# Optimization experiments

Measured on AMD Instinct MI355X. Metric: run time of the kernel, lower is better.

## Reference

```python
import jax, jax.numpy as jnp
import numpy as np

BOX_W, GIOU_W, OBJ_W, CLS_W, CTR_W = 5.0, 2.0, 1.0, 1.5, 0.5
POS_RADIUS = 1.0


def _bce_logits(x, t):
    # numerically stable binary cross entropy with logits
    return jnp.maximum(x, 0.0) - x * t + jnp.log1p(jnp.exp(-jnp.abs(x)))


def _focal(logits, targets, alpha=0.25, gamma=2.0):
    p = jax.nn.sigmoid(logits)
    ce = _bce_logits(logits, targets)
    p_t = p * targets + (1.0 - p) * (1.0 - targets)
    a_t = alpha * targets + (1.0 - alpha) * (1.0 - targets)
    return (a_t * ce * (1.0 - p_t) ** gamma).mean()


def _centerness(ltrb):
    l, t, r, b = ltrb[..., 0], ltrb[..., 1], ltrb[..., 2], ltrb[..., 3]
    hor = jnp.minimum(l, r) / jnp.maximum(jnp.maximum(l, r), 1e-6)
    ver = jnp.minimum(t, b) / jnp.maximum(jnp.maximum(t, b), 1e-6)
    return jnp.sqrt(jnp.maximum(hor * ver, 0.0))


def _build_targets(locations, gt_boxes, gt_labels, grid_h, grid_w, num_classes):
    # Vectorized equivalent of the sequential smallest-area-first assignment:
    # each location takes the smallest-area gt among its candidate gts.
    lx, ly = locations[:, 0], locations[:, 1]            # [L]
    cx, cy, w, h = (gt_boxes[..., i] for i in range(4))  # [B,M]
    x1, y1, x2, y2 = cx - w / 2, cy - h / 2, cx + w / 2, cy + h / 2
    area = w * h                                          # [B,M]
    # [B,M,L] booleans
    inside_box = (lx > x1[..., None]) & (ly > y1[..., None]) & (lx < x2[..., None]) & (ly < y2[..., None])
    rx, ry = POS_RADIUS / grid_w, POS_RADIUS / grid_h
    inside_center = (jnp.abs(lx - cx[..., None]) <= rx) & (jnp.abs(ly - cy[..., None]) <= ry)
    candidate = inside_box & inside_center
    # fallback: objects with no candidate grab the closest location (prefer inside-box)
    dist = (lx - cx[..., None]) ** 2 + (ly - cy[..., None]) ** 2
    dist_in = jnp.where(inside_box, dist, jnp.inf)
    best = jnp.where(inside_box.any(-1), jnp.argmin(dist_in, -1), jnp.argmin(dist, -1))  # [B,M]
    L = lx.shape[0]
    fallback = jax.nn.one_hot(best, L, dtype=bool)
    candidate = jnp.where(candidate.any(-1, keepdims=True), candidate, fallback)
    # per-location: pick candidate gt with min area (first index on ties)
    cost = jnp.where(candidate, area[..., None], jnp.inf)   # [B,M,L]
    assigned = jnp.argmin(cost, axis=1)                      # [B,L]
    positive = jnp.isfinite(jnp.min(cost, axis=1))           # [B,L]
    gt_xyxy = jnp.stack([x1, y1, x2, y2], axis=-1)           # [B,M,4]
    abox = jnp.take_along_axis(gt_xyxy, assigned[:, :, None], axis=1)  # [B,L,4]
    ltrb = jnp.stack([lx - abox[..., 0], ly - abox[..., 1], abox[..., 2] - lx, abox[..., 3] - ly], axis=-1)
    ltrb = jnp.maximum(ltrb, 1e-6)
    pos_f = positive.astype(jnp.float32)
    alab = jnp.take_along_axis(gt_labels, assigned, axis=1)  # [B,L]
    cls_t = jax.nn.one_hot(alab, num_classes, dtype=jnp.float32) * pos_f[..., None]
    ctr_t = _centerness(ltrb) * pos_f
    return abox * pos_f[..., None], ltrb * pos_f[..., None], cls_t, pos_f, ctr_t, positive


def _detection_loss(boxes_xyxy, box_deltas, class_logits, objectness, centerness,
                    locations, gt_boxes, gt_labels, grid_h, grid_w):
    C = class_logits.shape[-1]
    box_t, ltrb_t, cls_t, obj_t, ctr_t, positive = _build_targets(
        locations, gt_boxes, gt_labels, grid_h, grid_w, C)
    loss_obj = _focal(objectness, obj_t)
    loss_cls = _focal(class_logits, cls_t)
    # positive-weighted box terms (masked weighted sums over the full grid)
    weights = jnp.where(positive, jnp.maximum(jax.lax.stop_gradient(ctr_t), 0.1), 0.0)  # [B,L]
    wsum = weights.sum()
    # smooth L1 on ltrb deltas, beta=0.1
    beta = 0.1
    d = jnp.abs(box_deltas - ltrb_t)
    l1 = jnp.where(d < beta, 0.5 * d * d / beta, d - 0.5 * beta).mean(-1)  # [B,L]
    loss_l1 = (l1 * weights).sum() / wsum
    # elementwise GIoU between predicted and assigned gt xyxy boxes
    p, g = boxes_xyxy, box_t
    inter_lt = jnp.maximum(p[..., :2], g[..., :2])
    inter_rb = jnp.minimum(p[..., 2:], g[..., 2:])
    inter_wh = jnp.maximum(inter_rb - inter_lt, 0.0)
    inter = inter_wh[..., 0] * inter_wh[..., 1]
    area_p = jnp.maximum(p[..., 2] - p[..., 0], 0.0) * jnp.maximum(p[..., 3] - p[..., 1], 0.0)
    area_g = jnp.maximum(g[..., 2] - g[..., 0], 0.0) * jnp.maximum(g[..., 3] - g[..., 1], 0.0)
    union = area_p + area_g - inter
    iou = inter / jnp.maximum(union, 1e-6)
    hull_lt = jnp.minimum(p[..., :2], g[..., :2])
    hull_rb = jnp.maximum(p[..., 2:], g[..., 2:])
    hull_wh = jnp.maximum(hull_rb - hull_lt, 0.0)
    hull = hull_wh[..., 0] * hull_wh[..., 1]
    giou = iou - (hull - union) / jnp.maximum(hull, 1e-6)
    loss_giou = ((1.0 - giou) * weights).sum() / wsum
    ctr_bce = _bce_logits(centerness, ctr_t)
    loss_ctr = (ctr_bce * weights).sum() / wsum
    return (OBJ_W * loss_obj + CTR_W * loss_ctr + CLS_W * loss_cls
            + BOX_W * loss_l1 + GIOU_W * loss_giou)


def setup_inputs() -> dict:
    key = jax.random.key(0)
    ks = jax.random.split(key, 8)
    B, M, H, W, C = 16, 32, 128, 128, 80
    L = H * W
    ys, xs = jnp.meshgrid(jnp.arange(H, dtype=jnp.float32), jnp.arange(W, dtype=jnp.float32), indexing='ij')
    locations = jnp.stack([(xs + 0.5) / W, (ys + 0.5) / H], axis=-1).reshape(L, 2)
    gt_c = jax.random.uniform(ks[0], (B, M, 2), minval=0.1, maxval=0.9)
    gt_wh = jax.random.uniform(ks[1], (B, M, 2), minval=0.02, maxval=0.3)
    gt_boxes = jnp.concatenate([gt_c, gt_wh], axis=-1)
    gt_labels = jax.random.randint(ks[2], (B, M), 0, C)
    pc = jax.random.uniform(ks[3], (B, L, 2), minval=0.05, maxval=0.95)
    pwh = jax.random.uniform(ks[4], (B, L, 2), minval=0.02, maxval=0.3)
    boxes_xyxy = jnp.concatenate([pc - pwh / 2, pc + pwh / 2], axis=-1)
    box_deltas = jax.random.uniform(ks[5], (B, L, 4), minval=1e-3, maxval=0.3)
    class_logits = jax.random.normal(ks[6], (B, L, C), dtype=jnp.float32)
    k7, k8 = jax.random.split(ks[7])
    objectness = jax.random.normal(k7, (B, L), dtype=jnp.float32)
    centerness = jax.random.normal(k8, (B, L), dtype=jnp.float32)
    return {"boxes_xyxy": boxes_xyxy, "box_deltas": box_deltas, "class_logits": class_logits,
            "objectness": objectness, "centerness": centerness, "locations": locations,
            "gt_boxes": gt_boxes, "gt_labels": gt_labels, "grid_h": H, "grid_w": W}


def reference(boxes_xyxy, box_deltas, class_logits, objectness, centerness,
              locations, gt_boxes, gt_labels, grid_h, grid_w):
    return _detection_loss(boxes_xyxy, box_deltas, class_logits, objectness, centerness,
                           locations, gt_boxes, gt_labels, grid_h, grid_w)
```

## Files before the change

### kernel.cpp

```cpp
#include <hip/hip_runtime.h>
#include <cstdint>
#include <cstddef>
#include <math.h>

#define BOX_W_C  5.0f
#define GIOU_W_C 2.0f
#define OBJ_W_C  1.0f
#define CLS_W_C  1.5f
#define CTR_W_C  0.5f
#define POS_RADIUS_C 1.0f
#define MAXM 128
#define BLK 256

__device__ __forceinline__ float focal_elem(float x, float t) {
    float ax = fabsf(x);
    float e  = __expf(-ax);
    float lg = __logf(1.0f + e);
    float ce = fmaxf(x, 0.0f) - x * t + lg;
    float inv = 1.0f / (1.0f + e);
    float p  = (x >= 0.0f) ? inv : e * inv;
    float p_t = p * t + (1.0f - p) * (1.0f - t);
    float a_t = 0.25f * t + 0.75f * (1.0f - t);
    float om  = 1.0f - p_t;
    return a_t * ce * om * om;
}

__device__ __forceinline__ float focal_neg(float x) {
    float ax = fabsf(x);
    float e  = __expf(-ax);
    float lg = __logf(1.0f + e);
    float ce = fmaxf(x, 0.0f) + lg;
    float inv = 1.0f / (1.0f + e);
    float p  = (x >= 0.0f) ? inv : e * inv;
    return 0.75f * ce * p * p;
}

__device__ __forceinline__ float focal_pos_correction(float x) {
    float ax = fabsf(x);
    float e  = __expf(-ax);
    float lg = __logf(1.0f + e);
    float relu = fmaxf(x, 0.0f);
    float inv = 1.0f / (1.0f + e);
    float p  = (x >= 0.0f) ? inv : e * inv;
    float om = 1.0f - p;
    float f1 = 0.25f * (relu - x + lg) * om * om;
    float f0 = 0.75f * (relu + lg) * p * p;
    return f1 - f0;
}

__global__ void gt_assign_kernel(const float* __restrict__ locations,
                                 const float* __restrict__ gt_boxes,
                                 const int* __restrict__ gh_p,
                                 const int* __restrict__ gw_p,
                                 int L, int M,
                                 float* __restrict__ info,
                                 int* __restrict__ flags) {
    int bm  = blockIdx.x;
    int tid = threadIdx.x;

    const float* gb = gt_boxes + (size_t)bm * 4;
    float cx = gb[0], cy = gb[1], w = gb[2], h = gb[3];
    float x1 = cx - w * 0.5f, y1 = cy - h * 0.5f;
    float x2 = cx + w * 0.5f, y2 = cy + h * 0.5f;
    float area = w * h;
    float rx = POS_RADIUS_C / (float)gw_p[0];
    float ry = POS_RADIUS_C / (float)gh_p[0];

    float bin_v  = INFINITY; int bin_i  = 0x7fffffff;
    float ball_v = INFINITY; int ball_i = 0x7fffffff;
    int any_cand = 0, any_in = 0;

    const float2* loc2 = (const float2*)locations;
    for (int l = tid; l < L; l += blockDim.x) {
        float2 p2 = loc2[l];
        float lx = p2.x, ly = p2.y;
        bool inb = (lx > x1) && (ly > y1) && (lx < x2) && (ly < y2);
        bool inc = (fabsf(lx - cx) <= rx) && (fabsf(ly - cy) <= ry);
        any_cand |= (int)(inb && inc);
        any_in   |= (int)inb;
        float dx = lx - cx, dy = ly - cy;
        float dist = dx * dx + dy * dy;
        if (dist < ball_v) { ball_v = dist; ball_i = l; }
        float din = inb ? dist : INFINITY;
        if (din < bin_v) { bin_v = din; bin_i = l; }
    }

    __shared__ float s_v1[512]; __shared__ int s_i1[512];
    __shared__ float s_v2[512]; __shared__ int s_i2[512];
    __shared__ int s_c[512]; __shared__ int s_n[512];
    s_v1[tid] = bin_v;  s_i1[tid] = bin_i;
    s_v2[tid] = ball_v; s_i2[tid] = ball_i;
    s_c[tid] = any_cand; s_n[tid] = any_in;
    __syncthreads();
    for (int s = blockDim.x / 2; s > 0; s >>= 1) {
        if (tid < s) {
            if (s_v1[tid + s] < s_v1[tid] ||
                (s_v1[tid + s] == s_v1[tid] && s_i1[tid + s] < s_i1[tid])) {
                s_v1[tid] = s_v1[tid + s]; s_i1[tid] = s_i1[tid + s];
            }
            if (s_v2[tid + s] < s_v2[tid] ||
                (s_v2[tid + s] == s_v2[tid] && s_i2[tid + s] < s_i2[tid])) {
                s_v2[tid] = s_v2[tid + s]; s_i2[tid] = s_i2[tid + s];
            }
            s_c[tid] |= s_c[tid + s];
            s_n[tid] |= s_n[tid + s];
        }
        __syncthreads();
    }
    if (tid == 0) {
        int best = s_n[0] ? s_i1[0] : s_i2[0];
        flags[bm * 2]     = s_c[0];
        flags[bm * 2 + 1] = best;
        float* oi = info + (size_t)bm * 8;
        oi[0] = x1; oi[1] = y1; oi[2] = x2; oi[3] = y2;
        oi[4] = cx; oi[5] = cy; oi[6] = area; oi[7] = 0.0f;
    }
}

__global__ void fused_loss_kernel(const float* __restrict__ boxes_xyxy,
                                  const float* __restrict__ box_deltas,
                                  const float* __restrict__ class_logits,
                                  const float* __restrict__ objectness,
                                  const float* __restrict__ centerness,
                                  const float* __restrict__ locations,
                                  const int* __restrict__ gt_labels,
                                  const int* __restrict__ gh_p,
                                  const int* __restrict__ gw_p,
                                  int L, int M, int C, int bpb, int nblk,
                                  const float* __restrict__ info,
                                  const int* __restrict__ flags,
                                  float* __restrict__ partials) {
    __shared__ float s_x1[MAXM], s_y1[MAXM], s_x2[MAXM], s_y2[MAXM];
    __shared__ float s_cx[MAXM], s_cy[MAXM], s_area[MAXM];
    __shared__ int   s_lab[MAXM], s_hc[MAXM], s_best[MAXM];

    int b    = blockIdx.x / bpb;
    int lblk = blockIdx.x % bpb;
    int tid  = threadIdx.x;

    if (tid < M && tid < MAXM) {
        int bm = b * M + tid;
        const float* oi = info + (size_t)bm * 8;
        s_x1[tid] = oi[0]; s_y1[tid] = oi[1]; s_x2[tid] = oi[2]; s_y2[tid] = oi[3];
        s_cx[tid] = oi[4]; s_cy[tid] = oi[5]; s_area[tid] = oi[6];
        s_lab[tid]  = gt_labels[bm];
        s_hc[tid]   = flags[bm * 2];
        s_best[tid] = flags[bm * 2 + 1];
    }
    __syncthreads();

    int l0 = lblk * BLK;
    int l  = l0 + tid;
    float a_obj = 0.f, a_w = 0.f, a_l1 = 0.f, a_giou = 0.f, a_ctr = 0.f;
    float a_cls = 0.f;
    int mylab = -1;

    if (l < L) {
        size_t bl = (size_t)b * L + l;
        const float2* loc2 = (const float2*)locations;
        float2 p2 = loc2[l];
        float lx = p2.x, ly = p2.y;
        float rx = POS_RADIUS_C / (float)gw_p[0];
        float ry = POS_RADIUS_C / (float)gh_p[0];

        float minc = INFINITY;
        int   asg  = -1;
        for (int m = 0; m < M; ++m) {
            bool cand;
            if (s_hc[m]) {
                cand = (lx > s_x1[m]) && (ly > s_y1[m]) && (lx < s_x2[m]) && (ly < s_y2[m])
                    && (fabsf(lx - s_cx[m]) <= rx) && (fabsf(ly - s_cy[m]) <= ry);
            } else {
                cand = (l == s_best[m]);
            }
            if (cand && (s_area[m] < minc)) { minc = s_area[m]; asg = m; }
        }
        bool  pos   = (asg >= 0);
        float pos_f = pos ? 1.0f : 0.0f;
        mylab = pos ? s_lab[asg] : -1;

        a_obj = focal_elem(objectness[bl], pos_f);

        if (pos) {
            float ax1 = s_x1[asg], ay1 = s_y1[asg], ax2 = s_x2[asg], ay2 = s_y2[asg];
            float ltl = fmaxf(lx - ax1, 1e-6f);
            float ltt = fmaxf(ly - ay1, 1e-6f);
            float ltr = fmaxf(ax2 - lx, 1e-6f);
            float ltb = fmaxf(ay2 - ly, 1e-6f);
            float hor = fminf(ltl, ltr) / fmaxf(fmaxf(ltl, ltr), 1e-6f);
            float ver = fminf(ltt, ltb) / fmaxf(fmaxf(ltt, ltb), 1e-6f);
            float ctr_t = sqrtf(fmaxf(hor * ver, 0.0f));
            float wgt = fmaxf(ctr_t, 0.1f);
            a_w = wgt;

            const float4 bd = *(const float4*)(box_deltas + bl * 4);
            float d0 = fabsf(bd.x - ltl), d1 = fabsf(bd.y - ltt);
            float d2 = fabsf(bd.z - ltr), d3 = fabsf(bd.w - ltb);
            float l1s = ((d0 < 0.1f) ? (0.5f * d0 * d0 / 0.1f) : (d0 - 0.05f))
                      + ((d1 < 0.1f) ? (0.5f * d1 * d1 / 0.1f) : (d1 - 0.05f))
                      + ((d2 < 0.1f) ? (0.5f * d2 * d2 / 0.1f) : (d2 - 0.05f))
                      + ((d3 < 0.1f) ? (0.5f * d3 * d3 / 0.1f) : (d3 - 0.05f));
            a_l1 = (l1s * 0.25f) * wgt;

            const float4 pb = *(const float4*)(boxes_xyxy + bl * 4);
            float px1 = pb.x, py1 = pb.y, px2 = pb.z, py2 = pb.w;
            float ilx = fmaxf(px1, ax1), ily = fmaxf(py1, ay1);
            float irx = fminf(px2, ax2), iry = fminf(py2, ay2);
            float iw = fmaxf(irx - ilx, 0.f), ih = fmaxf(iry - ily, 0.f);
            float inter = iw * ih;
            float ap = fmaxf(px2 - px1, 0.f) * fmaxf(py2 - py1, 0.f);
            float ag = fmaxf(ax2 - ax1, 0.f) * fmaxf(ay2 - ay1, 0.f);
            float un = ap + ag - inter;
            float iou = inter / fmaxf(un, 1e-6f);
            float hlx = fminf(px1, ax1), hly = fminf(py1, ay1);
            float hrx = fmaxf(px2, ax2), hry = fmaxf(py2, ay2);
            float hw = fmaxf(hrx - hlx, 0.f), hh = fmaxf(hry - hly, 0.f);
            float hull = hw * hh;
            float giou = iou - (hull - un) / fmaxf(hull, 1e-6f);
            a_giou = (1.0f - giou) * wgt;

            float xc = centerness[bl];
            float bce = fmaxf(xc, 0.f) - xc * ctr_t + __logf(1.0f + __expf(-fabsf(xc)));
            a_ctr = bce * wgt;
        }

        if (mylab >= 0) {
            float xl = class_logits[bl * (size_t)C + mylab];
            a_cls += focal_pos_correction(xl);
        }
    }

    {
        int nrows = L - l0; if (nrows > BLK) nrows = BLK;
        int C4 = C >> 2;
        if (C4 > 0) {
            const float4* cl4 = (const float4*)(class_logits + ((size_t)b * L + l0) * C);
            int total4 = nrows * C4;
            for (int it = tid; it < total4; it += BLK) {
                float4 v = cl4[it];
                a_cls += focal_neg(v.x);
                a_cls += focal_neg(v.y);
                a_cls += focal_neg(v.z);
                a_cls += focal_neg(v.w);
            }
        }
        int crem = C - (C4 << 2);
        if (crem) {
            const float* base = class_logits + ((size_t)b * L + l0) * C + (C4 << 2);
            for (int rr = tid; rr < nrows; rr += BLK)
                for (int j = 0; j < crem; ++j)
                    a_cls += focal_neg(base[(size_t)rr * C + j]);
        }
    }

    for (int off = 32; off > 0; off >>= 1) {
        a_obj  += __shfl_down(a_obj,  off);
        a_w    += __shfl_down(a_w,    off);
        a_l1   += __shfl_down(a_l1,   off);
        a_giou += __shfl_down(a_giou, off);
        a_ctr  += __shfl_down(a_ctr,  off);
        a_cls  += __shfl_down(a_cls,  off);
    }
    __shared__ float red[BLK / 64][6];
    int wid = tid >> 6;
    if ((tid & 63) == 0) {
        red[wid][0] = a_obj; red[wid][1] = a_w; red[wid][2] = a_l1;
        red[wid][3] = a_giou; red[wid][4] = a_ctr; red[wid][5] = a_cls;
    }
    __syncthreads();
    if (tid == 0) {
        float r0 = 0.f, r1 = 0.f, r2 = 0.f, r3 = 0.f, r4 = 0.f, r5 = 0.f;
        for (int w2 = 0; w2 < BLK / 64; ++w2) {
            r0 += red[w2][0]; r1 += red[w2][1]; r2 += red[w2][2];
            r3 += red[w2][3]; r4 += red[w2][4]; r5 += red[w2][5];
        }
        int blk = (int)blockIdx.x;
        partials[0 * nblk + blk] = r0;
        partials[1 * nblk + blk] = r1;
        partials[2 * nblk + blk] = r2;
        partials[3 * nblk + blk] = r3;
        partials[4 * nblk + blk] = r4;
        partials[5 * nblk + blk] = r5;
    }
}

__global__ void finalize_kernel(const float* __restrict__ partials, int nblk,
                                float* __restrict__ out,
                                float invBL, float invBLC) {
    int tid = threadIdx.x;
    float r[6] = {0.f, 0.f, 0.f, 0.f, 0.f, 0.f};
    for (int i = tid; i < nblk; i += blockDim.x) {
        r[0] += partials[0 * nblk + i];
        r[1] += partials[1 * nblk + i];
        r[2] += partials[2 * nblk + i];
        r[3] += partials[3 * nblk + i];
        r[4] += partials[4 * nblk + i];
        r[5] += partials[5 * nblk + i];
    }
    __shared__ float red[256][6];
    for (int j = 0; j < 6; ++j) red[tid][j] = r[j];
    __syncthreads();
    for (int s = (int)blockDim.x / 2; s > 0; s >>= 1) {
        if (tid < s) {
            for (int j = 0; j < 6; ++j) red[tid][j] += red[tid + s][j];
        }
        __syncthreads();
    }
    if (tid == 0) {
        float obj  = red[0][0] * invBL;
        float wsum = red[0][1];
        float l1   = red[0][2] / wsum;
        float giou = red[0][3] / wsum;
        float ctr  = red[0][4] / wsum;
        float cls  = red[0][5] * invBLC;
        out[0] = OBJ_W_C * obj + CTR_W_C * ctr + CLS_W_C * cls + BOX_W_C * l1 + GIOU_W_C * giou;
    }
}

extern "C" void kernel_launch(void* const* d_in, const int* in_sizes, int n_in,
                              void* d_out, int out_size, void* d_ws, size_t ws_size,
                              hipStream_t stream) {
    const float* boxes_xyxy   = (const float*)d_in[0];
    const float* box_deltas   = (const float*)d_in[1];
    const float* class_logits = (const float*)d_in[2];
    const float* objectness   = (const float*)d_in[3];
    const float* centerness   = (const float*)d_in[4];
    const float* locations    = (const float*)d_in[5];
    const float* gt_boxes     = (const float*)d_in[6];
    const int*   gt_labels    = (const int*)d_in[7];
    const int*   gh           = (const int*)d_in[8];
    const int*   gw           = (const int*)d_in[9];

    int L = in_sizes[5] / 2;
    int B = in_sizes[3] / L;
    int C = in_sizes[2] / in_sizes[3];
    int M = in_sizes[7] / B;

    int bpb  = (L + BLK - 1) / BLK;
    int nblk = B * bpb;

    char* p = (char*)d_ws;
    int*   flags  = (int*)p;              p += ((size_t)B * M * 2 * sizeof(int) + 63) / 64 * 64;
    float* info   = (float*)p;            p += ((size_t)B * M * 8 * sizeof(float) + 63) / 64 * 64;
    float* partials = (float*)p;

    gt_assign_kernel<<<B * M, 512, 0, stream>>>(locations, gt_boxes, gh, gw,
                                                L, M, info, flags);

    fused_loss_kernel<<<nblk, BLK, 0, stream>>>(boxes_xyxy, box_deltas,
                                                class_logits, objectness,
                                                centerness, locations,
                                                gt_labels, gh, gw,
                                                L, M, C, bpb, nblk,
                                                info, flags, partials);

    float invBL  = (float)(1.0 / ((double)B * (double)L));
    float invBLC = (float)(1.0 / ((double)B * (double)L * (double)C));
    finalize_kernel<<<1, 256, 0, stream>>>(partials, nblk, (float*)d_out,
                                           invBL, invBLC);
}
```

Before: 175.8 us.

## Fuse finalize into loss kernel via atomic counter; wave-shuffle packed argmin in assign

```diff
diff --git a/kernel.cpp b/kernel.cpp
--- a/kernel.cpp
+++ b/kernel.cpp
@@ -11,6 +11,8 @@
 #define POS_RADIUS_C 1.0f
 #define MAXM 128
 #define BLK 256
+
+typedef float f4v __attribute__((ext_vector_type(4)));
 
 __device__ __forceinline__ float focal_elem(float x, float t) {
     float ax = fabsf(x);
@@ -48,15 +50,23 @@
     return f1 - f0;
 }
 
+__device__ __forceinline__ unsigned long long u64min(unsigned long long a,
+                                                     unsigned long long b) {
+    return (b < a) ? b : a;
+}
+
 __global__ void gt_assign_kernel(const float* __restrict__ locations,
                                  const float* __restrict__ gt_boxes,
                                  const int* __restrict__ gh_p,
                                  const int* __restrict__ gw_p,
                                  int L, int M,
                                  float* __restrict__ info,
-                                 int* __restrict__ flags) {
+                                 int* __restrict__ flags,
+                                 int* __restrict__ counter) {
     int bm  = blockIdx.x;
     int tid = threadIdx.x;
+
+    if (bm == 0 && tid == 0) *counter = 0;
 
     const float* gb = gt_boxes + (size_t)bm * 4;
     float cx = gb[0], cy = gb[1], w = gb[2], h = gb[3];
@@ -66,12 +76,12 @@
     float rx = POS_RADIUS_C / (float)gw_p[0];
     float ry = POS_RADIUS_C / (float)gh_p[0];
 
-    float bin_v  = INFINITY; int bin_i  = 0x7fffffff;
-    float ball_v = INFINITY; int ball_i = 0x7fffffff;
+    unsigned long long k_in  = ~0ull;
+    unsigned long long k_all = ~0ull;
     int any_cand = 0, any_in = 0;
 
     const float2* loc2 = (const float2*)locations;
-    for (int l = tid; l < L; l += blockDim.x) {
+    for (int l = tid; l < L; l += BLK) {
         float2 p2 = loc2[l];
         float lx = p2.x, ly = p2.y;
         bool inb = (lx > x1) && (ly > y1) && (lx < x2) && (ly < y2);
@@ -80,36 +90,38 @@
         any_in   |= (int)inb;
         float dx = lx - cx, dy = ly - cy;
         float dist = dx * dx + dy * dy;
-        if (dist < ball_v) { ball_v = dist; ball_i = l; }
-        float din = inb ? dist : INFINITY;
-        if (din < bin_v) { bin_v = din; bin_i = l; }
-    }
-
-    __shared__ float s_v1[512]; __shared__ int s_i1[512];
-    __shared__ float s_v2[512]; __shared__ int s_i2[512];
-    __shared__ int s_c[512]; __shared__ int s_n[512];
-    s_v1[tid] = bin_v;  s_i1[tid] = bin_i;
-    s_v2[tid] = ball_v; s_i2[tid] = ball_i;
-    s_c[tid] = any_cand; s_n[tid] = any_in;
-    __syncthreads();
-    for (int s = blockDim.x / 2; s > 0; s >>= 1) {
-        if (tid < s) {
-            if (s_v1[tid + s] < s_v1[tid] ||
-                (s_v1[tid + s] == s_v1[tid] && s_i1[tid + s] < s_i1[tid])) {
-                s_v1[tid] = s_v1[tid + s]; s_i1[tid] = s_i1[tid + s];
-            }
-            if (s_v2[tid + s] < s_v2[tid] ||
-                (s_v2[tid + s] == s_v2[tid] && s_i2[tid + s] < s_i2[tid])) {
-                s_v2[tid] = s_v2[tid + s]; s_i2[tid] = s_i2[tid + s];
-            }
-            s_c[tid] |= s_c[tid + s];
-            s_n[tid] |= s_n[tid + s];
-        }
-        __syncthreads();
-    }
+        unsigned long long kd =
+            ((unsigned long long)__float_as_uint(dist) << 32) | (unsigned)l;
+        k_all = u64min(k_all, kd);
+        if (inb) k_in = u64min(k_in, kd);
+    }
+
+    for (int off = 32; off > 0; off >>= 1) {
+        unsigned long long o1 = __shfl_down(k_in,  off);
+        unsigned long long o2 = __shfl_down(k_all, off);
+        k_in  = u64min(k_in,  o1);
+        k_all = u64min(k_all, o2);
+        any_cand |= __shfl_down(any_cand, off);
+        any_in   |= __shfl_down(any_in,   off);
+    }
+
+    __shared__ unsigned long long sk1[BLK / 64], sk2[BLK / 64];
+    __shared__ int sc[BLK / 64], sn[BLK / 64];
+    int wid = tid >> 6;
+    if ((tid & 63) == 0) {
+        sk1[wid] = k_in; sk2[wid] = k_all;
+        sc[wid] = any_cand; sn[wid] = any_in;
+    }
+    __syncthreads();
     if (tid == 0) {
-        int best = s_n[0] ? s_i1[0] : s_i2[0];
-        flags[bm * 2]     = s_c[0];
+        for (int w2 = 1; w2 < BLK / 64; ++w2) {
+            k_in  = u64min(k_in,  sk1[w2]);
+            k_all = u64min(k_all, sk2[w2]);
+            any_cand |= sc[w2];
+            any_in   |= sn[w2];
+        }
+        int best = any_in ? (int)(k_in & 0xffffffffu) : (int)(k_all & 0xffffffffu);
+        flags[bm * 2]     = any_cand;
         flags[bm * 2 + 1] = best;
         float* oi = info + (size_t)bm * 8;
         oi[0] = x1; oi[1] = y1; oi[2] = x2; oi[3] = y2;
@@ -129,7 +141,10 @@
                                   int L, int M, int C, int bpb, int nblk,
                                   const float* __restrict__ info,
                                   const int* __restrict__ flags,
-                                  float* __restrict__ partials) {
+                                  float* __restrict__ partials,
+                                  int* __restrict__ counter,
+                                  float* __restrict__ out,
+                                  float invBL, float invBLC) {
     __shared__ float s_x1[MAXM], s_y1[MAXM], s_x2[MAXM], s_y2[MAXM];
     __shared__ float s_cx[MAXM], s_cy[MAXM], s_area[MAXM];
     __shared__ int   s_lab[MAXM], s_hc[MAXM], s_best[MAXM];
@@ -234,14 +249,15 @@
         int nrows = L - l0; if (nrows > BLK) nrows = BLK;
         int C4 = C >> 2;
         if (C4 > 0) {
-            const float4* cl4 = (const float4*)(class_logits + ((size_t)b * L + l0) * C);
+            const f4v* cl4 = (const f4v*)(class_logits + ((size_t)b * L + l0) * C);
             int total4 = nrows * C4;
+            #pragma unroll 2
             for (int it = tid; it < total4; it += BLK) {
-                float4 v = cl4[it];
-                a_cls += focal_neg(v.x);
-                a_cls += focal_neg(v.y);
-                a_cls += focal_neg(v.z);
-                a_cls += focal_neg(v.w);
+                f4v v = __builtin_nontemporal_load(cl4 + it);
+                a_cls += focal_neg(v[0]);
+                a_cls += focal_neg(v[1]);
+                a_cls += focal_neg(v[2]);
+                a_cls += focal_neg(v[3]);
             }
         }
         int crem = C - (C4 << 2);
@@ -262,6 +278,7 @@
         a_cls  += __shfl_down(a_cls,  off);
     }
     __shared__ float red[BLK / 64][6];
+    __shared__ int s_last;
     int wid = tid >> 6;
     if ((tid & 63) == 0) {
         red[wid][0] = a_obj; red[wid][1] = a_w; red[wid][2] = a_l1;
@@ -281,15 +298,16 @@
         partials[3 * nblk + blk] = r3;
         partials[4 * nblk + blk] = r4;
         partials[5 * nblk + blk] = r5;
-    }
-}
-
-__global__ void finalize_kernel(const float* __restrict__ partials, int nblk,
-                                float* __restrict__ out,
-                                float invBL, float invBLC) {
-    int tid = threadIdx.x;
+        int done = __hip_atomic_fetch_add(counter, 1, __ATOMIC_ACQ_REL,
+                                          __HIP_MEMORY_SCOPE_AGENT);
+        s_last = (done == nblk - 1) ? 1 : 0;
+    }
+    __syncthreads();
+    if (!s_last) return;
+
+    __threadfence();
     float r[6] = {0.f, 0.f, 0.f, 0.f, 0.f, 0.f};
-    for (int i = tid; i < nblk; i += blockDim.x) {
+    for (int i = tid; i < nblk; i += BLK) {
         r[0] += partials[0 * nblk + i];
         r[1] += partials[1 * nblk + i];
         r[2] += partials[2 * nblk + i];
@@ -297,22 +315,22 @@
         r[4] += partials[4 * nblk + i];
         r[5] += partials[5 * nblk + i];
     }
-    __shared__ float red[256][6];
-    for (int j = 0; j < 6; ++j) red[tid][j] = r[j];
-    __syncthreads();
-    for (int s = (int)blockDim.x / 2; s > 0; s >>= 1) {
+    __shared__ float fred[BLK][6];
+    for (int j = 0; j < 6; ++j) fred[tid][j] = r[j];
+    __syncthreads();
+    for (int s = BLK / 2; s > 0; s >>= 1) {
         if (tid < s) {
-            for (int j = 0; j < 6; ++j) red[tid][j] += red[tid + s][j];
+            for (int j = 0; j < 6; ++j) fred[tid][j] += fred[tid + s][j];
         }
         __syncthreads();
     }
     if (tid == 0) {
-        float obj  = red[0][0] * invBL;
-        float wsum = red[0][1];
-        float l1   = red[0][2] / wsum;
-        float giou = red[0][3] / wsum;
-        float ctr  = red[0][4] / wsum;
-        float cls  = red[0][5] * invBLC;
+        float obj  = fred[0][0] * invBL;
+        float wsum = fred[0][1];
+        float l1   = fred[0][2] / wsum;
+        float giou = fred[0][3] / wsum;
+        float ctr  = fred[0][4] / wsum;
+        float cls  = fred[0][5] * invBLC;
         out[0] = OBJ_W_C * obj + CTR_W_C * ctr + CLS_W_C * cls + BOX_W_C * l1 + GIOU_W_C * giou;
     }
 }
@@ -342,20 +360,21 @@
     char* p = (char*)d_ws;
     int*   flags  = (int*)p;              p += ((size_t)B * M * 2 * sizeof(int) + 63) / 64 * 64;
     float* info   = (float*)p;            p += ((size_t)B * M * 8 * sizeof(float) + 63) / 64 * 64;
-    float* partials = (float*)p;
-
-    gt_assign_kernel<<<B * M, 512, 0, stream>>>(locations, gt_boxes, gh, gw,
-                                                L, M, info, flags);
+    float* partials = (float*)p;          p += ((size_t)6 * nblk * sizeof(float) + 63) / 64 * 64;
+    int*   counter = (int*)p;
+
+    gt_assign_kernel<<<B * M, BLK, 0, stream>>>(locations, gt_boxes, gh, gw,
+                                                L, M, info, flags, counter);
+
+    float invBL  = (float)(1.0 / ((double)B * (double)L));
+    float invBLC = (float)(1.0 / ((double)B * (double)L * (double)C));
 
     fused_loss_kernel<<<nblk, BLK, 0, stream>>>(boxes_xyxy, box_deltas,
                                                 class_logits, objectness,
                                                 centerness, locations,
                                                 gt_labels, gh, gw,
                                                 L, M, C, bpb, nblk,
-                                                info, flags, partials);
-
-    float invBL  = (float)(1.0 / ((double)B * (double)L));
-    float invBLC = (float)(1.0 / ((double)B * (double)L * (double)C));
-    finalize_kernel<<<1, 256, 0, stream>>>(partials, nblk, (float*)d_out,
-                                           invBL, invBLC);
-}
+                                                info, flags, partials,
+                                                counter, (float*)d_out,
+                                                invBL, invBLC);
+}
```

Measured after the change: 224.7 us. 1.28x slower.
